# Kernel tuning notes

Hardware: AMD Instinct MI355X
Metric: run time of the kernel (lower is better)

## Reference

```python
import jax, jax.numpy as jnp
import numpy as np

B, N, IN_F = 16, 1024, 256
HEADS, OUT_F = 4, 64
NEG_SLOPE = 0.2
CLAMP_MIN = -1e9
MASK_VAL = -9e15


def setup_inputs() -> dict:
    key = jax.random.key(0)
    k1, k2, k3, k4 = jax.random.split(key, 4)
    x = jax.random.normal(k1, (B, N, IN_F), dtype=jnp.float32)
    adj = jax.random.randint(k2, (B, N, N), 0, 2, dtype=jnp.int32)
    # Linear weight, stored as (in, heads*out) so y = x @ W (xavier-uniform scale)
    lim_w = float(np.sqrt(6.0 / (IN_F + HEADS * OUT_F)))
    W = jax.random.uniform(k3, (IN_F, HEADS * OUT_F), dtype=jnp.float32,
                           minval=-lim_w, maxval=lim_w)
    lim_a = float(np.sqrt(6.0 / (2 * OUT_F + HEADS)))
    a = jax.random.uniform(k4, (2 * OUT_F, HEADS), dtype=jnp.float32,
                           minval=-lim_a, maxval=lim_a)
    return {"x": x, "adj": adj, "W": W, "a": a}


def reference(x, adj, W, a):
    Bs, Ns, _ = x.shape
    # Projection: (B,N,H,D)
    h = (x @ W).reshape(Bs, Ns, HEADS, OUT_F)
    # cat([h_i, h_j]) . a == h_i . a_src + h_j . a_dst  (exact same math, no O(N^2*2D) tensor)
    a_src, a_dst = a[:OUT_F], a[OUT_F:]          # each (D, H)
    s_src = jnp.einsum('bnhd,dh->bnh', h, a_src)  # score contribution of node i
    s_dst = jnp.einsum('bnhd,dh->bnh', h, a_dst)  # score contribution of node j
    e = jax.nn.leaky_relu(s_src[:, :, None, :] + s_dst[:, None, :, :],
                          negative_slope=NEG_SLOPE)  # (B,N,N,H)
    # match original: subtract unmasked row max, clamp, then mask, then softmax over j
    e = e - jnp.max(e, axis=2, keepdims=True)
    e = jnp.maximum(e, CLAMP_MIN)
    att = jnp.where(adj[..., None] > 0, e, MASK_VAL)
    att = jax.nn.softmax(att, axis=2)
    h_prime = jnp.einsum('bijh,bjhd->bihd', att, h)  # (B,N,H,D)
    return h_prime.reshape(Bs, Ns, HEADS * OUT_F)
```

## Files before the change

kernel.cpp:

```cpp
#include <hip/hip_runtime.h>
#include <hip/hip_bf16.h>

#define B_   16
#define N_   1024
#define INF_ 256
#define NH_  4
#define HD_  256
#define L2E  1.4426950408889634f

typedef __attribute__((ext_vector_type(8))) short short8;
typedef __attribute__((ext_vector_type(4))) float f32x4;

__device__ __forceinline__ float bf2f(unsigned short u) {
    union { unsigned int i; float f; } v; v.i = ((unsigned int)u) << 16; return v.f;
}
__device__ __forceinline__ unsigned short f2bf(float f) {
    union { float f; unsigned int i; } v; v.f = f;
    unsigned int x = v.i;
    return (unsigned short)((x + 0x7fffu + ((x >> 16) & 1u)) >> 16);
}

__global__ __launch_bounds__(256) void k_prepw(const float* __restrict__ W,
                                               unsigned short* __restrict__ wswz)
{
    int slot = blockIdx.x * 256 + threadIdx.x;
    int kstep = slot >> 10;
    int nt    = (slot >> 6) & 15;
    int lane  = slot & 63;
    int k0 = kstep * 32 + (lane >> 4) * 8;
    int n  = nt * 16 + (lane & 15);
    ushort4 o0, o1;
    o0.x = f2bf(W[(k0 + 0) * HD_ + n]);
    o0.y = f2bf(W[(k0 + 1) * HD_ + n]);
    o0.z = f2bf(W[(k0 + 2) * HD_ + n]);
    o0.w = f2bf(W[(k0 + 3) * HD_ + n]);
    o1.x = f2bf(W[(k0 + 4) * HD_ + n]);
    o1.y = f2bf(W[(k0 + 5) * HD_ + n]);
    o1.z = f2bf(W[(k0 + 6) * HD_ + n]);
    o1.w = f2bf(W[(k0 + 7) * HD_ + n]);
    *(ushort4*)&wswz[(long)slot * 8]     = o0;
    *(ushort4*)&wswz[(long)slot * 8 + 4] = o1;
}

__global__ __launch_bounds__(256) void k_gemm_h(
    const float* __restrict__ x, const float* __restrict__ a,
    const unsigned short* __restrict__ wswz,
    unsigned short* __restrict__ hswz,
    float* __restrict__ ssrc, float* __restrict__ sdst)
{
    __shared__ unsigned short xls[16][264];
    int t = threadIdx.x;
    int blk = blockIdx.x;
    int row0 = blk * 16;
    int b  = blk >> 6;
    int n0 = row0 & 1023;

    {
        int sr = t >> 4, sc = (t & 15) * 16;
        const float* xp = x + (long)(row0 + sr) * INF_ + sc;
        float4 v0 = ((const float4*)xp)[0];
        float4 v1 = ((const float4*)xp)[1];
        float4 v2 = ((const float4*)xp)[2];
        float4 v3 = ((const float4*)xp)[3];
        ushort4 u0 = {f2bf(v0.x), f2bf(v0.y), f2bf(v0.z), f2bf(v0.w)};
        ushort4 u1 = {f2bf(v1.x), f2bf(v1.y), f2bf(v1.z), f2bf(v1.w)};
        ushort4 u2 = {f2bf(v2.x), f2bf(v2.y), f2bf(v2.z), f2bf(v2.w)};
        ushort4 u3 = {f2bf(v3.x), f2bf(v3.y), f2bf(v3.z), f2bf(v3.w)};
        *(ushort4*)&xls[sr][sc]      = u0;
        *(ushort4*)&xls[sr][sc + 4]  = u1;
        *(ushort4*)&xls[sr][sc + 8]  = u2;
        *(ushort4*)&xls[sr][sc + 12] = u3;
    }
    __syncthreads();

    int wave = t >> 6, lane = t & 63, quad = lane >> 4, l15 = lane & 15;
    f32x4 acc[4];
    #pragma unroll
    for (int i = 0; i < 4; i++) acc[i] = (f32x4){0.f, 0.f, 0.f, 0.f};

    #pragma unroll
    for (int ks = 0; ks < 8; ks++) {
        short8 af = *(const short8*)&xls[l15][ks * 32 + quad * 8];
        #pragma unroll
        for (int nt = 0; nt < 4; nt++) {
            short8 bf = *(const short8*)(wswz +
                ((long)((ks * 16 + wave * 4 + nt) * 64 + lane)) * 8);
            acc[nt] = __builtin_amdgcn_mfma_f32_16x16x32_bf16(af, bf, acc[nt], 0, 0, 0);
        }
    }

    int q0 = (quad & 1) * 4;
    int qd = ((row0 & 31) + quad * 4) >> 3;
    long bj32 = row0 >> 5;
    #pragma unroll
    for (int nt = 0; nt < 4; nt++) {
        int dg = wave * 4 + nt;
        long idx8 = (bj32 * 16 + dg) * 64 + qd * 16 + l15;
        ushort4 o = {f2bf(acc[nt][0]), f2bf(acc[nt][1]),
                     f2bf(acc[nt][2]), f2bf(acc[nt][3])};
        *(ushort4*)&hswz[idx8 * 8 + q0] = o;
    }

    float as_[4], ad_[4];
    #pragma unroll
    for (int nt = 0; nt < 4; nt++) {
        int d = nt * 16 + l15;
        as_[nt] = a[d * NH_ + wave];
        ad_[nt] = a[(64 + d) * NH_ + wave];
    }
    #pragma unroll
    for (int r = 0; r < 4; r++) {
        float ps = acc[0][r] * as_[0] + acc[1][r] * as_[1]
                 + acc[2][r] * as_[2] + acc[3][r] * as_[3];
        float pd = acc[0][r] * ad_[0] + acc[1][r] * ad_[1]
                 + acc[2][r] * ad_[2] + acc[3][r] * ad_[3];
        #pragma unroll
        for (int m = 1; m < 16; m <<= 1) {
            ps += __shfl_xor(ps, m);
            pd += __shfl_xor(pd, m);
        }
        if (l15 == 0) {
            int row = n0 + quad * 4 + r;
            ssrc[((long)b * NH_ + wave) * N_ + row] = ps * L2E;
            sdst[((long)b * NH_ + wave) * N_ + row] = pd * L2E;
        }
    }
}

__global__ __launch_bounds__(512) void k_attn(
    const int* __restrict__ adj, const unsigned short* __restrict__ hswz,
    const float* __restrict__ ssrc, const float* __restrict__ sdst,
    float* __restrict__ out)
{
    __shared__ unsigned int maskw[16][33];
    __shared__ float ss_s[4][16];
    __shared__ float accb[4][64][20];

    int t = threadIdx.x;
    int b  = blockIdx.x >> 6, it = blockIdx.x & 63;
    int i0 = it * 16;
    int wave = t >> 6, lane = t & 63, quad = lane >> 4, l15 = lane & 15;
    int hh = wave & 3, jh = wave >> 2;

    {
        int row = t >> 5, w = t & 31;
        const int4* ar = (const int4*)(adj + (((long)b * N_ + i0 + row) << 10) + w * 32);
        unsigned int u = 0;
        #pragma unroll
        for (int k = 0; k < 8; k++) {
            int4 av = ar[k];
            u |= ((unsigned)av.x) << (4 * k);
            u |= ((unsigned)av.y) << (4 * k + 1);
            u |= ((unsigned)av.z) << (4 * k + 2);
            u |= ((unsigned)av.w) << (4 * k + 3);
        }
        maskw[row][w] = u;
    }
    if (t < 64) {
        int h = t >> 4, i = t & 15;
        ss_s[h][i] = ssrc[((long)(b * NH_ + h)) * N_ + i0 + i];
    }
    __syncthreads();

    float ssi = ss_s[hh][l15];
    const float* sdp = sdst + ((long)(b * NH_ + hh)) * N_ + jh * 512;

    f32x4 acc[4], dn;
    #pragma unroll
    for (int i = 0; i < 4; i++) acc[i] = (f32x4){0.f, 0.f, 0.f, 0.f};
    dn = (f32x4){0.f, 0.f, 0.f, 0.f};
    short8 ones;
    #pragma unroll
    for (int i = 0; i < 8; i++) ones[i] = (short)0x3F80;

    int shq = quad * 8;

    #pragma unroll 4
    for (int jc = 0; jc < 16; jc++) {
        unsigned int byv = (maskw[l15][jh * 16 + jc] >> shq) & 0xffu;
        const float* sj = sdp + jc * 32 + quad * 8;
        float4 sA = *(const float4*)sj;
        float4 sB = *(const float4*)(sj + 4);
        float sv[8] = {sA.x, sA.y, sA.z, sA.w, sB.x, sB.y, sB.z, sB.w};

        union { unsigned int u[4]; short8 s; } pk;
        #pragma unroll
        for (int qp = 0; qp < 4; qp++) {
            unsigned int wb[2];
            #pragma unroll
            for (int hv = 0; hv < 2; hv++) {
                int q = 2 * qp + hv;
                float e = ssi + sv[q];
                float w = __builtin_exp2f(fmaxf(e, 0.2f * e));
                w = ((byv >> q) & 1u) ? w : 0.f;
                wb[hv] = __float_as_uint(w) + 0x8000u;
            }
            pk.u[qp] = (wb[1] & 0xffff0000u) | (wb[0] >> 16);
        }

        long s8 = ((long)(b * 32 + jh * 16 + jc)) * 1024;
        #pragma unroll
        for (int idt = 0; idt < 4; idt++) {
            short8 bf = *(const short8*)(hswz + (s8 + (hh * 4 + idt) * 64 + lane) * 8);
            acc[idt] = __builtin_amdgcn_mfma_f32_16x16x32_bf16(pk.s, bf, acc[idt], 0, 0, 0);
        }
        dn = __builtin_amdgcn_mfma_f32_16x16x32_bf16(pk.s, ones, dn, 0, 0, 0);
    }

    if (jh == 1) {
        #pragma unroll
        for (int idt = 0; idt < 4; idt++)
            *(f32x4*)&accb[hh][lane][idt * 4] = acc[idt];
        *(f32x4*)&accb[hh][lane][16] = dn;
    }
    __syncthreads();

    if (jh == 0) {
        f32x4 od = *(const f32x4*)&accb[hh][lane][16];
        float inv[4];
        #pragma unroll
        for (int r = 0; r < 4; r++)
            inv[r] = 1.0f / (dn[r] + od[r]);
        #pragma unroll
        for (int idt = 0; idt < 4; idt++) {
            f32x4 o = *(const f32x4*)&accb[hh][lane][idt * 4];
            int col = hh * 64 + idt * 16 + l15;
            #pragma unroll
            for (int r = 0; r < 4; r++) {
                long row_g = (long)b * N_ + i0 + quad * 4 + r;
                out[row_g * HD_ + col] = (acc[idt][r] + o[r]) * inv[r];
            }
        }
    }
}

extern "C" void kernel_launch(void* const* d_in, const int* in_sizes, int n_in,
                              void* d_out, int out_size, void* d_ws, size_t ws_size,
                              hipStream_t stream) {
    const float* x   = (const float*)d_in[0];
    const int*   adj = (const int*)d_in[1];
    const float* W   = (const float*)d_in[2];
    const float* a   = (const float*)d_in[3];
    float* out = (float*)d_out;

    unsigned short* hswz = (unsigned short*)d_ws;
    unsigned short* wswz = hswz + (long)B_ * N_ * HD_;
    float* ssrc = (float*)(wswz + INF_ * HD_);
    float* sdst = ssrc + (long)B_ * NH_ * N_;

    k_prepw<<<32, 256, 0, stream>>>(W, wswz);
    k_gemm_h<<<1024, 256, 0, stream>>>(x, a, wswz, hswz, ssrc, sdst);
    k_attn<<<1024, 512, 0, stream>>>(adj, hswz, ssrc, sdst, out);
}
```

Before: 173.6 us.

## Pre-pack adjacency into bitmask in prep kernel; simplify attention to single j-pass

The int32 adjacency-to-bitmask packing moves out of the attention kernel into the prep kernel, which uses wave ballots, and the result goes to a global bitmask buffer. The attention kernel then reads compact mask words directly. It drops its LDS staging, barriers and the two-wave j-split reduction and uses 256-thread blocks that each cover all j. This separates the bandwidth-heavy 64MB adj read from the MFMA-heavy attention loop. In exchange it adds an extra global write/read of the packed mask and halves per-block parallelism in the attention stage.

```diff
diff --git a/kernel.cpp b/kernel.cpp
--- a/kernel.cpp
+++ b/kernel.cpp
@@ -19,27 +19,61 @@
     unsigned int x = v.i;
     return (unsigned short)((x + 0x7fffu + ((x >> 16) & 1u)) >> 16);
 }
-
-__global__ __launch_bounds__(256) void k_prepw(const float* __restrict__ W,
-                                               unsigned short* __restrict__ wswz)
+__device__ __forceinline__ unsigned int spread4(unsigned int x) {
+    x = (x | (x << 12)) & 0x000F000Fu;
+    x = (x | (x << 6))  & 0x03030303u;
+    x = (x | (x << 3))  & 0x11111111u;
+    return x;
+}
+
+__global__ __launch_bounds__(256) void k_prep(const int* __restrict__ adj,
+                                              const float* __restrict__ W,
+                                              unsigned int* __restrict__ pb,
+                                              unsigned short* __restrict__ wswz)
 {
-    int slot = blockIdx.x * 256 + threadIdx.x;
-    int kstep = slot >> 10;
-    int nt    = (slot >> 6) & 15;
-    int lane  = slot & 63;
-    int k0 = kstep * 32 + (lane >> 4) * 8;
-    int n  = nt * 16 + (lane & 15);
-    ushort4 o0, o1;
-    o0.x = f2bf(W[(k0 + 0) * HD_ + n]);
-    o0.y = f2bf(W[(k0 + 1) * HD_ + n]);
-    o0.z = f2bf(W[(k0 + 2) * HD_ + n]);
-    o0.w = f2bf(W[(k0 + 3) * HD_ + n]);
-    o1.x = f2bf(W[(k0 + 4) * HD_ + n]);
-    o1.y = f2bf(W[(k0 + 5) * HD_ + n]);
-    o1.z = f2bf(W[(k0 + 6) * HD_ + n]);
-    o1.w = f2bf(W[(k0 + 7) * HD_ + n]);
-    *(ushort4*)&wswz[(long)slot * 8]     = o0;
-    *(ushort4*)&wswz[(long)slot * 8 + 4] = o1;
+    int bx = blockIdx.x, t = threadIdx.x;
+    if (bx < 512) {
+        int wave = t >> 6, lane = t & 63;
+        int row0 = (bx * 4 + wave) * 8;
+        for (int r8 = 0; r8 < 8; r8++) {
+            int row = row0 + r8;
+            const int4* ar = (const int4*)(adj + ((long)row << 10));
+            #pragma unroll
+            for (int rd = 0; rd < 4; rd++) {
+                int4 av = ar[rd * 64 + lane];
+                unsigned long long b0 = __ballot(av.x);
+                unsigned long long b1 = __ballot(av.y);
+                unsigned long long b2 = __ballot(av.z);
+                unsigned long long b3 = __ballot(av.w);
+                if (lane < 8) {
+                    int sh = lane * 8;
+                    unsigned int w =  spread4((unsigned int)(b0 >> sh) & 0xffu)
+                                   | (spread4((unsigned int)(b1 >> sh) & 0xffu) << 1)
+                                   | (spread4((unsigned int)(b2 >> sh) & 0xffu) << 2)
+                                   | (spread4((unsigned int)(b3 >> sh) & 0xffu) << 3);
+                    pb[((long)row << 5) + rd * 8 + lane] = w;
+                }
+            }
+        }
+    } else {
+        int slot = (bx - 512) * 256 + t;
+        int kstep = slot >> 10;
+        int nt    = (slot >> 6) & 15;
+        int lane  = slot & 63;
+        int k0 = kstep * 32 + (lane >> 4) * 8;
+        int n  = nt * 16 + (lane & 15);
+        ushort4 o0, o1;
+        o0.x = f2bf(W[(k0 + 0) * HD_ + n]);
+        o0.y = f2bf(W[(k0 + 1) * HD_ + n]);
+        o0.z = f2bf(W[(k0 + 2) * HD_ + n]);
+        o0.w = f2bf(W[(k0 + 3) * HD_ + n]);
+        o1.x = f2bf(W[(k0 + 4) * HD_ + n]);
+        o1.y = f2bf(W[(k0 + 5) * HD_ + n]);
+        o1.z = f2bf(W[(k0 + 6) * HD_ + n]);
+        o1.w = f2bf(W[(k0 + 7) * HD_ + n]);
+        *(ushort4*)&wswz[(long)slot * 8]     = o0;
+        *(ushort4*)&wswz[(long)slot * 8 + 4] = o1;
+    }
 }
 
 __global__ __launch_bounds__(256) void k_gemm_h(
@@ -127,43 +161,20 @@
     }
 }
 
-__global__ __launch_bounds__(512) void k_attn(
-    const int* __restrict__ adj, const unsigned short* __restrict__ hswz,
+__global__ __launch_bounds__(256) void k_attn(
+    const unsigned int* __restrict__ pb, const unsigned short* __restrict__ hswz,
     const float* __restrict__ ssrc, const float* __restrict__ sdst,
     float* __restrict__ out)
 {
-    __shared__ unsigned int maskw[16][33];
-    __shared__ float ss_s[4][16];
-    __shared__ float accb[4][64][20];
-
     int t = threadIdx.x;
     int b  = blockIdx.x >> 6, it = blockIdx.x & 63;
     int i0 = it * 16;
-    int wave = t >> 6, lane = t & 63, quad = lane >> 4, l15 = lane & 15;
-    int hh = wave & 3, jh = wave >> 2;
-
-    {
-        int row = t >> 5, w = t & 31;
-        const int4* ar = (const int4*)(adj + (((long)b * N_ + i0 + row) << 10) + w * 32);
-        unsigned int u = 0;
-        #pragma unroll
-        for (int k = 0; k < 8; k++) {
-            int4 av = ar[k];
-            u |= ((unsigned)av.x) << (4 * k);
-            u |= ((unsigned)av.y) << (4 * k + 1);
-            u |= ((unsigned)av.z) << (4 * k + 2);
-            u |= ((unsigned)av.w) << (4 * k + 3);
-        }
-        maskw[row][w] = u;
-    }
-    if (t < 64) {
-        int h = t >> 4, i = t & 15;
-        ss_s[h][i] = ssrc[((long)(b * NH_ + h)) * N_ + i0 + i];
-    }
-    __syncthreads();
-
-    float ssi = ss_s[hh][l15];
-    const float* sdp = sdst + ((long)(b * NH_ + hh)) * N_ + jh * 512;
+    int hh = t >> 6, lane = t & 63, quad = lane >> 4, l15 = lane & 15;
+    int shq = quad * 8;
+
+    float ssi = ssrc[((long)(b * NH_ + hh)) * N_ + i0 + l15];
+    const float* sdp = sdst + ((long)(b * NH_ + hh)) * N_;
+    const unsigned int* pbrow = pb + (((long)(b * N_ + i0 + l15)) << 5);
 
     f32x4 acc[4], dn;
     #pragma unroll
@@ -173,63 +184,56 @@
     #pragma unroll
     for (int i = 0; i < 8; i++) ones[i] = (short)0x3F80;
 
-    int shq = quad * 8;
-
     #pragma unroll 4
-    for (int jc = 0; jc < 16; jc++) {
-        unsigned int byv = (maskw[l15][jh * 16 + jc] >> shq) & 0xffu;
-        const float* sj = sdp + jc * 32 + quad * 8;
-        float4 sA = *(const float4*)sj;
-        float4 sB = *(const float4*)(sj + 4);
-        float sv[8] = {sA.x, sA.y, sA.z, sA.w, sB.x, sB.y, sB.z, sB.w};
-
-        union { unsigned int u[4]; short8 s; } pk;
-        #pragma unroll
-        for (int qp = 0; qp < 4; qp++) {
-            unsigned int wb[2];
+    for (int jq = 0; jq < 8; jq++) {
+        uint4 mq = *(const uint4*)(pbrow + jq * 4);
+        #pragma unroll
+        for (int js = 0; js < 4; js++) {
+            int jc = jq * 4 + js;
+            unsigned int mw = (js == 0) ? mq.x : (js == 1) ? mq.y
+                             : (js == 2) ? mq.z : mq.w;
+            unsigned int byv = (mw >> shq) & 0xffu;
+
+            const float* sj = sdp + jc * 32 + quad * 8;
+            float4 sA = *(const float4*)sj;
+            float4 sB = *(const float4*)(sj + 4);
+            float sv[8] = {sA.x, sA.y, sA.z, sA.w, sB.x, sB.y, sB.z, sB.w};
+
+            union { unsigned int u[4]; short8 s; } pk;
             #pragma unroll
-            for (int hv = 0; hv < 2; hv++) {
-                int q = 2 * qp + hv;
-                float e = ssi + sv[q];
-                float w = __builtin_exp2f(fmaxf(e, 0.2f * e));
-                w = ((byv >> q) & 1u) ? w : 0.f;
-                wb[hv] = __float_as_uint(w) + 0x8000u;
+            for (int qp = 0; qp < 4; qp++) {
+                unsigned int wb[2];
+                #pragma unroll
+                for (int hv = 0; hv < 2; hv++) {
+                    int q = 2 * qp + hv;
+                    float e = ssi + sv[q];
+                    float w = __builtin_exp2f(fmaxf(e, 0.2f * e));
+                    w = ((byv >> q) & 1u) ? w : 0.f;
+                    wb[hv] = __float_as_uint(w) + 0x8000u;
+                }
+                pk.u[qp] = (wb[1] & 0xffff0000u) | (wb[0] >> 16);
             }
-            pk.u[qp] = (wb[1] & 0xffff0000u) | (wb[0] >> 16);
-        }
-
-        long s8 = ((long)(b * 32 + jh * 16 + jc)) * 1024;
-        #pragma unroll
-        for (int idt = 0; idt < 4; idt++) {
-            short8 bf = *(const short8*)(hswz + (s8 + (hh * 4 + idt) * 64 + lane) * 8);
-            acc[idt] = __builtin_amdgcn_mfma_f32_16x16x32_bf16(pk.s, bf, acc[idt], 0, 0, 0);
-        }
-        dn = __builtin_amdgcn_mfma_f32_16x16x32_bf16(pk.s, ones, dn, 0, 0, 0);
-    }
-
-    if (jh == 1) {
-        #pragma unroll
-        for (int idt = 0; idt < 4; idt++)
-            *(f32x4*)&accb[hh][lane][idt * 4] = acc[idt];
-        *(f32x4*)&accb[hh][lane][16] = dn;
-    }
-    __syncthreads();
-
-    if (jh == 0) {
-        f32x4 od = *(const f32x4*)&accb[hh][lane][16];
-        float inv[4];
-        #pragma unroll
-        for (int r = 0; r < 4; r++)
-            inv[r] = 1.0f / (dn[r] + od[r]);
-        #pragma unroll
-        for (int idt = 0; idt < 4; idt++) {
-            f32x4 o = *(const f32x4*)&accb[hh][lane][idt * 4];
-            int col = hh * 64 + idt * 16 + l15;
+
+            long s8 = ((long)(b * 32 + jc)) * 1024;
             #pragma unroll
-            for (int r = 0; r < 4; r++) {
-                long row_g = (long)b * N_ + i0 + quad * 4 + r;
-                out[row_g * HD_ + col] = (acc[idt][r] + o[r]) * inv[r];
+            for (int idt = 0; idt < 4; idt++) {
+                short8 bf = *(const short8*)(hswz + (s8 + (hh * 4 + idt) * 64 + lane) * 8);
+                acc[idt] = __builtin_amdgcn_mfma_f32_16x16x32_bf16(pk.s, bf, acc[idt], 0, 0, 0);
             }
+            dn = __builtin_amdgcn_mfma_f32_16x16x32_bf16(pk.s, ones, dn, 0, 0, 0);
+        }
+    }
+
+    float inv[4];
+    #pragma unroll
+    for (int r = 0; r < 4; r++) inv[r] = 1.0f / dn[r];
+    #pragma unroll
+    for (int idt = 0; idt < 4; idt++) {
+        int col = hh * 64 + idt * 16 + l15;
+        #pragma unroll
+        for (int r = 0; r < 4; r++) {
+            long row_g = (long)b * N_ + i0 + quad * 4 + r;
+            out[row_g * HD_ + col] = acc[idt][r] * inv[r];
         }
     }
 }
@@ -243,12 +247,13 @@
     const float* a   = (const float*)d_in[3];
     float* out = (float*)d_out;
 
-    unsigned short* hswz = (unsigned short*)d_ws;
-    unsigned short* wswz = hswz + (long)B_ * N_ * HD_;
+    unsigned int* pb      = (unsigned int*)d_ws;
+    unsigned short* hswz  = (unsigned short*)(pb + 524288);
+    unsigned short* wswz  = hswz + (long)B_ * N_ * HD_;
     float* ssrc = (float*)(wswz + INF_ * HD_);
     float* sdst = ssrc + (long)B_ * NH_ * N_;
 
-    k_prepw<<<32, 256, 0, stream>>>(W, wswz);
+    k_prep<<<544, 256, 0, stream>>>(adj, W, pb, wswz);
     k_gemm_h<<<1024, 256, 0, stream>>>(x, a, wswz, hswz, ssrc, sdst);
-    k_attn<<<1024, 512, 0, stream>>>(adj, hswz, ssrc, sdst, out);
-}
+    k_attn<<<1024, 256, 0, stream>>>(pb, hswz, ssrc, sdst, out);
+}
```

After: 172.4 us. No clear change (-0.7%).

## Factor exp of leaky-relu scores into per-node products and prepack adjacency bits

Applied to the files above, without the earlier changes.

The per-pair exp2 of the leaky-relu score is replaced by max(Pi*Pj, Qi*Qj), using exponentials of the source and destination scores and their 0.2-scaled versions. These are precomputed once per node in the GEMM epilogue, so the attention inner loop needs only multiplies and a max instead of one transcendental per element. Adjacency bit-packing moves into a separate prep kernel merged with the W prep, so the attention kernel loads packed mask words directly and no longer needs its shared-memory prologue and barrier. In exchange there are extra workspace round trips for the packed mask and four score arrays, and the products can overflow for large scores where the old exp2 of the sum stayed in range.

```diff
diff --git a/kernel.cpp b/kernel.cpp
--- a/kernel.cpp
+++ b/kernel.cpp
@@ -11,42 +11,60 @@
 typedef __attribute__((ext_vector_type(8))) short short8;
 typedef __attribute__((ext_vector_type(4))) float f32x4;
 
-__device__ __forceinline__ float bf2f(unsigned short u) {
-    union { unsigned int i; float f; } v; v.i = ((unsigned int)u) << 16; return v.f;
-}
 __device__ __forceinline__ unsigned short f2bf(float f) {
     union { float f; unsigned int i; } v; v.f = f;
     unsigned int x = v.i;
     return (unsigned short)((x + 0x7fffu + ((x >> 16) & 1u)) >> 16);
 }
 
-__global__ __launch_bounds__(256) void k_prepw(const float* __restrict__ W,
-                                               unsigned short* __restrict__ wswz)
+__global__ __launch_bounds__(256) void k_prep(const int* __restrict__ adj,
+                                              const float* __restrict__ W,
+                                              unsigned int* __restrict__ pb,
+                                              unsigned short* __restrict__ wswz)
 {
-    int slot = blockIdx.x * 256 + threadIdx.x;
-    int kstep = slot >> 10;
-    int nt    = (slot >> 6) & 15;
-    int lane  = slot & 63;
-    int k0 = kstep * 32 + (lane >> 4) * 8;
-    int n  = nt * 16 + (lane & 15);
-    ushort4 o0, o1;
-    o0.x = f2bf(W[(k0 + 0) * HD_ + n]);
-    o0.y = f2bf(W[(k0 + 1) * HD_ + n]);
-    o0.z = f2bf(W[(k0 + 2) * HD_ + n]);
-    o0.w = f2bf(W[(k0 + 3) * HD_ + n]);
-    o1.x = f2bf(W[(k0 + 4) * HD_ + n]);
-    o1.y = f2bf(W[(k0 + 5) * HD_ + n]);
-    o1.z = f2bf(W[(k0 + 6) * HD_ + n]);
-    o1.w = f2bf(W[(k0 + 7) * HD_ + n]);
-    *(ushort4*)&wswz[(long)slot * 8]     = o0;
-    *(ushort4*)&wswz[(long)slot * 8 + 4] = o1;
+    int bx = blockIdx.x, t = threadIdx.x;
+    if (bx < 2048) {
+        int g = bx * 256 + t;
+        int w   = g & 31;
+        int row = g >> 5;
+        const int* ar = adj + ((long)row << 10) + w * 32;
+        unsigned int u = 0;
+        #pragma unroll
+        for (int k = 0; k < 8; k++) {
+            int4 av = *(const int4*)(ar + k * 4);
+            u |= ((unsigned)av.x) << (4 * k);
+            u |= ((unsigned)av.y) << (4 * k + 1);
+            u |= ((unsigned)av.z) << (4 * k + 2);
+            u |= ((unsigned)av.w) << (4 * k + 3);
+        }
+        pb[g] = u;
+    } else {
+        int slot = (bx - 2048) * 256 + t;
+        int kstep = slot >> 10;
+        int nt    = (slot >> 6) & 15;
+        int lane  = slot & 63;
+        int k0 = kstep * 32 + (lane >> 4) * 8;
+        int n  = nt * 16 + (lane & 15);
+        ushort4 o0, o1;
+        o0.x = f2bf(W[(k0 + 0) * HD_ + n]);
+        o0.y = f2bf(W[(k0 + 1) * HD_ + n]);
+        o0.z = f2bf(W[(k0 + 2) * HD_ + n]);
+        o0.w = f2bf(W[(k0 + 3) * HD_ + n]);
+        o1.x = f2bf(W[(k0 + 4) * HD_ + n]);
+        o1.y = f2bf(W[(k0 + 5) * HD_ + n]);
+        o1.z = f2bf(W[(k0 + 6) * HD_ + n]);
+        o1.w = f2bf(W[(k0 + 7) * HD_ + n]);
+        *(ushort4*)&wswz[(long)slot * 8]     = o0;
+        *(ushort4*)&wswz[(long)slot * 8 + 4] = o1;
+    }
 }
 
 __global__ __launch_bounds__(256) void k_gemm_h(
     const float* __restrict__ x, const float* __restrict__ a,
     const unsigned short* __restrict__ wswz,
     unsigned short* __restrict__ hswz,
-    float* __restrict__ ssrc, float* __restrict__ sdst)
+    float* __restrict__ Ps, float* __restrict__ Qs,
+    float* __restrict__ Pd, float* __restrict__ Qd)
 {
     __shared__ unsigned short xls[16][264];
     int t = threadIdx.x;
@@ -121,19 +139,22 @@
         }
         if (l15 == 0) {
             int row = n0 + quad * 4 + r;
-            ssrc[((long)b * NH_ + wave) * N_ + row] = ps * L2E;
-            sdst[((long)b * NH_ + wave) * N_ + row] = pd * L2E;
-        }
-    }
-}
-
-__global__ __launch_bounds__(512) void k_attn(
-    const int* __restrict__ adj, const unsigned short* __restrict__ hswz,
-    const float* __restrict__ ssrc, const float* __restrict__ sdst,
+            long o = ((long)b * NH_ + wave) * N_ + row;
+            float ss = ps * L2E, sd = pd * L2E;
+            Ps[o] = __builtin_exp2f(ss);
+            Qs[o] = __builtin_exp2f(0.2f * ss);
+            Pd[o] = __builtin_exp2f(sd);
+            Qd[o] = __builtin_exp2f(0.2f * sd);
+        }
+    }
+}
+
+__global__ __launch_bounds__(512, 5) void k_attn(
+    const unsigned int* __restrict__ pb, const unsigned short* __restrict__ hswz,
+    const float* __restrict__ Ps, const float* __restrict__ Qs,
+    const float* __restrict__ Pd, const float* __restrict__ Qd,
     float* __restrict__ out)
 {
-    __shared__ unsigned int maskw[16][33];
-    __shared__ float ss_s[4][16];
     __shared__ float accb[4][64][20];
 
     int t = threadIdx.x;
@@ -142,28 +163,12 @@
     int wave = t >> 6, lane = t & 63, quad = lane >> 4, l15 = lane & 15;
     int hh = wave & 3, jh = wave >> 2;
 
-    {
-        int row = t >> 5, w = t & 31;
-        const int4* ar = (const int4*)(adj + (((long)b * N_ + i0 + row) << 10) + w * 32);
-        unsigned int u = 0;
-        #pragma unroll
-        for (int k = 0; k < 8; k++) {
-            int4 av = ar[k];
-            u |= ((unsigned)av.x) << (4 * k);
-            u |= ((unsigned)av.y) << (4 * k + 1);
-            u |= ((unsigned)av.z) << (4 * k + 2);
-            u |= ((unsigned)av.w) << (4 * k + 3);
-        }
-        maskw[row][w] = u;
-    }
-    if (t < 64) {
-        int h = t >> 4, i = t & 15;
-        ss_s[h][i] = ssrc[((long)(b * NH_ + h)) * N_ + i0 + i];
-    }
-    __syncthreads();
-
-    float ssi = ss_s[hh][l15];
-    const float* sdp = sdst + ((long)(b * NH_ + hh)) * N_ + jh * 512;
+    long bhN = ((long)(b * NH_ + hh)) * N_;
+    float Pi = Ps[bhN + i0 + l15];
+    float Qi = Qs[bhN + i0 + l15];
+    const float* Pdp = Pd + bhN + jh * 512;
+    const float* Qdp = Qd + bhN + jh * 512;
+    const unsigned int* pbrow = pb + (((long)(b * N_ + i0 + l15)) << 5) + jh * 16;
 
     f32x4 acc[4], dn;
     #pragma unroll
@@ -175,36 +180,46 @@
 
     int shq = quad * 8;
 
-    #pragma unroll 4
-    for (int jc = 0; jc < 16; jc++) {
-        unsigned int byv = (maskw[l15][jh * 16 + jc] >> shq) & 0xffu;
-        const float* sj = sdp + jc * 32 + quad * 8;
-        float4 sA = *(const float4*)sj;
-        float4 sB = *(const float4*)(sj + 4);
-        float sv[8] = {sA.x, sA.y, sA.z, sA.w, sB.x, sB.y, sB.z, sB.w};
-
-        union { unsigned int u[4]; short8 s; } pk;
-        #pragma unroll
-        for (int qp = 0; qp < 4; qp++) {
-            unsigned int wb[2];
+    #pragma unroll 2
+    for (int jq = 0; jq < 4; jq++) {
+        uint4 mq = *(const uint4*)(pbrow + jq * 4);
+        #pragma unroll
+        for (int js = 0; js < 4; js++) {
+            int jc = jq * 4 + js;
+            unsigned int mw = (js == 0) ? mq.x : (js == 1) ? mq.y
+                             : (js == 2) ? mq.z : mq.w;
+            unsigned int byv = (mw >> shq) & 0xffu;
+
+            const float* pj = Pdp + jc * 32 + quad * 8;
+            const float* qj = Qdp + jc * 32 + quad * 8;
+            float4 pA = *(const float4*)pj;
+            float4 pB = *(const float4*)(pj + 4);
+            float4 qA = *(const float4*)qj;
+            float4 qB = *(const float4*)(qj + 4);
+            float pv[8] = {pA.x, pA.y, pA.z, pA.w, pB.x, pB.y, pB.z, pB.w};
+            float qv[8] = {qA.x, qA.y, qA.z, qA.w, qB.x, qB.y, qB.z, qB.w};
+
+            union { unsigned int u[4]; short8 s; } pk;
             #pragma unroll
-            for (int hv = 0; hv < 2; hv++) {
-                int q = 2 * qp + hv;
-                float e = ssi + sv[q];
-                float w = __builtin_exp2f(fmaxf(e, 0.2f * e));
-                w = ((byv >> q) & 1u) ? w : 0.f;
-                wb[hv] = __float_as_uint(w) + 0x8000u;
+            for (int qp = 0; qp < 4; qp++) {
+                float w0 = fmaxf(Pi * pv[2 * qp],     Qi * qv[2 * qp]);
+                float w1 = fmaxf(Pi * pv[2 * qp + 1], Qi * qv[2 * qp + 1]);
+                w0 = ((byv >> (2 * qp))     & 1u) ? w0 : 0.f;
+                w1 = ((byv >> (2 * qp + 1)) & 1u) ? w1 : 0.f;
+                float2 f2 = make_float2(w0, w1);
+                __hip_bfloat162 bb = __float22bfloat162_rn(f2);
+                union { __hip_bfloat162 b; unsigned int u; } cv; cv.b = bb;
+                pk.u[qp] = cv.u;
             }
-            pk.u[qp] = (wb[1] & 0xffff0000u) | (wb[0] >> 16);
-        }
-
-        long s8 = ((long)(b * 32 + jh * 16 + jc)) * 1024;
-        #pragma unroll
-        for (int idt = 0; idt < 4; idt++) {
-            short8 bf = *(const short8*)(hswz + (s8 + (hh * 4 + idt) * 64 + lane) * 8);
-            acc[idt] = __builtin_amdgcn_mfma_f32_16x16x32_bf16(pk.s, bf, acc[idt], 0, 0, 0);
-        }
-        dn = __builtin_amdgcn_mfma_f32_16x16x32_bf16(pk.s, ones, dn, 0, 0, 0);
+
+            long s8 = ((long)(b * 32 + jh * 16 + jc)) * 1024;
+            #pragma unroll
+            for (int idt = 0; idt < 4; idt++) {
+                short8 bf = *(const short8*)(hswz + (s8 + (hh * 4 + idt) * 64 + lane) * 8);
+                acc[idt] = __builtin_amdgcn_mfma_f32_16x16x32_bf16(pk.s, bf, acc[idt], 0, 0, 0);
+            }
+            dn = __builtin_amdgcn_mfma_f32_16x16x32_bf16(pk.s, ones, dn, 0, 0, 0);
+        }
     }
 
     if (jh == 1) {
@@ -243,12 +258,15 @@
     const float* a   = (const float*)d_in[3];
     float* out = (float*)d_out;
 
-    unsigned short* hswz = (unsigned short*)d_ws;
-    unsigned short* wswz = hswz + (long)B_ * N_ * HD_;
-    float* ssrc = (float*)(wswz + INF_ * HD_);
-    float* sdst = ssrc + (long)B_ * NH_ * N_;
-
-    k_prepw<<<32, 256, 0, stream>>>(W, wswz);
-    k_gemm_h<<<1024, 256, 0, stream>>>(x, a, wswz, hswz, ssrc, sdst);
-    k_attn<<<1024, 512, 0, stream>>>(adj, hswz, ssrc, sdst, out);
-}
+    unsigned int* pb      = (unsigned int*)d_ws;
+    unsigned short* hswz  = (unsigned short*)(pb + 524288);
+    unsigned short* wswz  = hswz + (long)B_ * N_ * HD_;
+    float* Ps = (float*)(wswz + INF_ * HD_);
+    float* Qs = Ps + (long)B_ * NH_ * N_;
+    float* Pd = Qs + (long)B_ * NH_ * N_;
+    float* Qd = Pd + (long)B_ * NH_ * N_;
+
+    k_prep<<<2080, 256, 0, stream>>>(adj, W, pb, wswz);
+    k_gemm_h<<<1024, 256, 0, stream>>>(x, a, wswz, hswz, Ps, Qs, Pd, Qd);
+    k_attn<<<1024, 512, 0, stream>>>(pb, hswz, Ps, Qs, Pd, Qd, out);
+}
```

Measured after the change: 172.7 us. No clear change (-0.5%).
